# Performance work log

Measured on AMD Instinct MI355X. Metric: run time of the kernel, lower is better.

## Reference

```python
import jax, jax.numpy as jnp
import numpy as np

B, L, H, E = 2, 2048, 8, 64
S = L  # self-attention


def setup_inputs() -> dict:
    key = jax.random.key(0)
    k1, k2, k3, k4, k5 = jax.random.split(key, 5)
    return {
        "queries": jax.random.normal(k1, (B, L, H, E), dtype=jnp.float32),
        "keys": jax.random.normal(k2, (B, S, H, E), dtype=jnp.float32),
        "values": jax.random.normal(k3, (B, S, H, E), dtype=jnp.float32),
        "tau": jax.random.uniform(k4, (B, 1), dtype=jnp.float32),
        "delta": jax.random.normal(k5, (B, S), dtype=jnp.float32),
    }


def reference(queries, keys, values, tau, delta):
    # De-stationary attention: scores = (QK^T) * tau + delta, causal mask, softmax, AV
    E_ = queries.shape[-1]
    scale = 1.0 / jnp.sqrt(jnp.float32(E_))
    tau_b = tau[:, None, None, :]      # [B,1,1,1]
    delta_b = delta[:, None, None, :]  # [B,1,1,S]
    scores = jnp.einsum('blhe,bshe->bhls', queries, keys) * tau_b + delta_b  # [B,H,L,S]
    Lq, Sk = scores.shape[-2], scores.shape[-1]
    causal = jnp.triu(jnp.ones((Lq, Sk), dtype=bool), k=1)  # True = masked
    scores = jnp.where(causal[None, None], -jnp.inf, scores)
    A = jax.nn.softmax(scale * scores, axis=-1)
    V = jnp.einsum('bhls,bshd->blhd', A, values)
    return V
```

## Files before the change

kernel.cpp:

```cpp
#include <hip/hip_runtime.h>


typedef _Float16 h8 __attribute__((ext_vector_type(8)));
typedef _Float16 h2 __attribute__((ext_vector_type(2)));
typedef float f32x4 __attribute__((ext_vector_type(4)));

constexpr int Bc = 2, Lc = 2048, Hc = 8, Ec = 64, Sc = 2048;
constexpr int QT = 64, KT = 64;
constexpr int NQT = Lc / QT;
constexpr int LDK = 72;
constexpr float SCALE = 0.125f;
constexpr float LOG2E = 1.44269504088896340736f;

__device__ __forceinline__ h2 pk2(float x, float y) {
  return __builtin_bit_cast(h2, __builtin_amdgcn_cvt_pkrtz(x, y));
}

template <int CTRL>
__device__ __forceinline__ float dpp_f(float x) {
  int r = __builtin_amdgcn_update_dpp(0, __builtin_bit_cast(int, x), CTRL, 0xF, 0xF, true);
  return __builtin_bit_cast(float, r);
}
__device__ __forceinline__ float rowmax16(float x) {
  x = fmaxf(x, dpp_f<0xB1>(x));
  x = fmaxf(x, dpp_f<0x4E>(x));
  x = fmaxf(x, dpp_f<0x124>(x));
  x = fmaxf(x, dpp_f<0x128>(x));
  return x;
}

template <int CH, int EPB>
__global__ __launch_bounds__(256, 3)
void dsattn_fwd(const float* __restrict__ Qg, const float* __restrict__ Kg,
                const float* __restrict__ Vg, const float* __restrict__ taug,
                const float* __restrict__ deltag, float* __restrict__ Og,
                float* __restrict__ Opart, float* __restrict__ Mpart,
                float* __restrict__ Lpart) {
  __shared__ __align__(16) _Float16 Ks[2][KT * LDK];
  __shared__ __align__(16) _Float16 Vt[2][Ec * LDK];
  __shared__ __align__(16) _Float16 Pb[4][16 * LDK];

  const int bx = (int)blockIdx.x;
  int qt, c0;
  if (CH >= NQT) { qt = NQT - 1 - bx; c0 = 0; }
  else { qt = NQT - 1 - (bx >> 2); c0 = bx & 3; if (c0 * CH > qt) return; }
  const int nch = qt / CH + 1;
  const int ktBeg = c0 * CH;
  const int ktEnd = (qt < ktBeg + CH - 1) ? qt : (ktBeg + CH - 1);

  const int tid = threadIdx.x;
  const int wave = tid >> 6, lane = tid & 63;
  const int quad = lane >> 4, l16 = lane & 15;
  const int q0 = qt * QT;
  const int bh = (int)blockIdx.y;
  const int b = bh >> 3, h = bh & 7;

  const float ct = taug[b] * (SCALE * LOG2E);

  const int qm = q0 + (wave << 4) + l16;
  const float* qp = Qg + (((size_t)b * Lc + qm) * Hc + h) * Ec;
  h8 qfrag[2];
#pragma unroll
  for (int kk = 0; kk < 2; ++kk) {
    float4 a0 = ((const float4*)(qp + quad * 8 + kk * 32))[0];
    float4 a1 = ((const float4*)(qp + quad * 8 + kk * 32))[1];
    union { h8 v; h2 p[4]; } u;
    u.p[0] = pk2(a0.x, a0.y); u.p[1] = pk2(a0.z, a0.w);
    u.p[2] = pk2(a1.x, a1.y); u.p[3] = pk2(a1.z, a1.w);
    qfrag[kk] = u.v;
  }

  h8 onesf;
#pragma unroll
  for (int j = 0; j < 8; ++j) onesf[j] = (_Float16)1.0f;

  f32x4 Oacc[4], Osum;
#pragma unroll
  for (int nt = 0; nt < 4; ++nt) Oacc[nt] = (f32x4){0.f, 0.f, 0.f, 0.f};
  Osum = (f32x4){0.f, 0.f, 0.f, 0.f};
  float mrow[4];
#pragma unroll
  for (int r = 0; r < 4; ++r) mrow[r] = -1e30f;

  const int srow = tid >> 2;
  const int sec = (tid & 3) << 4;
  const int vrp = ((tid >> 3) + 4 * (tid & 7)) & 31;
  const int ve8 = (tid & 7) << 3;

  _Float16* pb = &Pb[wave][0];
  float dcur[4];

  {
    const int kb = ktBeg * KT;
    const float* kp = Kg + (((size_t)b * Sc + kb + srow) * Hc + h) * Ec + sec;
    float4 c0v = ((const float4*)kp)[0], c1v = ((const float4*)kp)[1];
    float4 c2v = ((const float4*)kp)[2], c3v = ((const float4*)kp)[3];
    const float* vp0 = Vg + (((size_t)b * Sc + kb + 2 * vrp) * Hc + h) * Ec + ve8;
    const float* vp1 = vp0 + Hc * Ec;
    float4 r00 = ((const float4*)vp0)[0], r01 = ((const float4*)vp0)[1];
    float4 r10 = ((const float4*)vp1)[0], r11 = ((const float4*)vp1)[1];
#pragma unroll
    for (int nt = 0; nt < 4; ++nt)
      dcur[nt] = deltag[(size_t)b * Sc + kb + nt * 16 + l16] * (SCALE * LOG2E);
    union { h8 v; h2 p[4]; } w0, w1;
    w0.p[0] = pk2(c0v.x, c0v.y); w0.p[1] = pk2(c0v.z, c0v.w);
    w0.p[2] = pk2(c1v.x, c1v.y); w0.p[3] = pk2(c1v.z, c1v.w);
    w1.p[0] = pk2(c2v.x, c2v.y); w1.p[1] = pk2(c2v.z, c2v.w);
    w1.p[2] = pk2(c3v.x, c3v.y); w1.p[3] = pk2(c3v.z, c3v.w);
    *(h8*)&Ks[0][srow * LDK + sec] = w0.v;
    *(h8*)&Ks[0][srow * LDK + sec + 8] = w1.v;
    const float e0[8] = {r00.x, r00.y, r00.z, r00.w, r01.x, r01.y, r01.z, r01.w};
    const float e1[8] = {r10.x, r10.y, r10.z, r10.w, r11.x, r11.y, r11.z, r11.w};
#pragma unroll
    for (int j = 0; j < 8; ++j)
      *(h2*)&Vt[0][(ve8 + j) * LDK + 2 * vrp] = pk2(e0[j], e1[j]);
  }

  for (int kt = ktBeg; kt <= ktEnd; ++kt) {
    const int cur = (kt - ktBeg) & 1;
    const bool pf = (kt < ktEnd);

    float4 kn0, kn1, kn2, kn3, vn00, vn01, vn10, vn11;
    float dn[4];
    if (pf) {
      const int nb = (kt + 1) * KT;
      const float* kp = Kg + (((size_t)b * Sc + nb + srow) * Hc + h) * Ec + sec;
      kn0 = ((const float4*)kp)[0]; kn1 = ((const float4*)kp)[1];
      kn2 = ((const float4*)kp)[2]; kn3 = ((const float4*)kp)[3];
      const float* vp0 = Vg + (((size_t)b * Sc + nb + 2 * vrp) * Hc + h) * Ec + ve8;
      const float* vp1 = vp0 + Hc * Ec;
      vn00 = ((const float4*)vp0)[0]; vn01 = ((const float4*)vp0)[1];
      vn10 = ((const float4*)vp1)[0]; vn11 = ((const float4*)vp1)[1];
#pragma unroll
      for (int nt = 0; nt < 4; ++nt)
        dn[nt] = deltag[(size_t)b * Sc + nb + nt * 16 + l16];
    }

    __syncthreads();

    f32x4 Sacc[4];
#pragma unroll
    for (int nt = 0; nt < 4; ++nt) Sacc[nt] = (f32x4){0.f, 0.f, 0.f, 0.f};
#pragma unroll
    for (int kk = 0; kk < 2; ++kk) {
#pragma unroll
      for (int nt = 0; nt < 4; ++nt) {
        h8 bf = *(const h8*)&Ks[cur][(nt * 16 + l16) * LDK + quad * 8 + kk * 32];
        Sacc[nt] = __builtin_amdgcn_mfma_f32_16x16x32_f16(qfrag[kk], bf, Sacc[nt], 0, 0, 0);
      }
    }

    const int kbase = kt * KT;
    const int qr0 = q0 + (wave << 4) + (quad << 2);
    const bool diag = (kt == qt);
    float sv[4][4];
#pragma unroll
    for (int nt = 0; nt < 4; ++nt) {
      const int key = kbase + nt * 16 + l16;
#pragma unroll
      for (int r = 0; r < 4; ++r) {
        float s = Sacc[nt][r] * ct + dcur[nt];
        sv[nt][r] = (!diag || key <= qr0 + r) ? s : -1e30f;
      }
    }

    float alpha[4];
#pragma unroll
    for (int r = 0; r < 4; ++r) {
      float t = fmaxf(fmaxf(sv[0][r], sv[1][r]), fmaxf(sv[2][r], sv[3][r]));
      t = rowmax16(t);
      float mn = fmaxf(mrow[r], t);
      alpha[r] = __builtin_amdgcn_exp2f(mrow[r] - mn);
      mrow[r] = mn;
    }
#pragma unroll
    for (int nt = 0; nt < 4; ++nt)
#pragma unroll
      for (int r = 0; r < 4; ++r)
        sv[nt][r] = __builtin_amdgcn_exp2f(sv[nt][r] - mrow[r]);

#pragma unroll
    for (int nt = 0; nt < 4; ++nt)
#pragma unroll
      for (int r = 0; r < 4; ++r) Oacc[nt][r] *= alpha[r];
#pragma unroll
    for (int r = 0; r < 4; ++r) Osum[r] *= alpha[r];

    {
      const int lo = l16 & 1;
      const int base = (lo ? 32 : 0) + (l16 & ~1);
#pragma unroll
      for (int r = 0; r < 4; ++r) {
        float o0 = dpp_f<0xB1>(sv[0][r]);
        float o1 = dpp_f<0xB1>(sv[1][r]);
        float o2 = dpp_f<0xB1>(sv[2][r]);
        float o3 = dpp_f<0xB1>(sv[3][r]);
        h2 d0 = pk2(lo ? o2 : sv[0][r], lo ? sv[2][r] : o0);
        h2 d1 = pk2(lo ? o3 : sv[1][r], lo ? sv[3][r] : o1);
        _Float16* pp = &pb[((quad << 2) + r) * LDK + base];
        *(h2*)pp = d0;
        *(h2*)(pp + 16) = d1;
      }
    }
    asm volatile("s_waitcnt lgkmcnt(0)" ::: "memory");

#pragma unroll
    for (int kk = 0; kk < 2; ++kk) {
      h8 af = *(const h8*)&pb[l16 * LDK + quad * 8 + kk * 32];
#pragma unroll
      for (int nt = 0; nt < 4; ++nt) {
        h8 vf = *(const h8*)&Vt[cur][(nt * 16 + l16) * LDK + quad * 8 + kk * 32];
        Oacc[nt] = __builtin_amdgcn_mfma_f32_16x16x32_f16(af, vf, Oacc[nt], 0, 0, 0);
      }
      Osum = __builtin_amdgcn_mfma_f32_16x16x32_f16(af, onesf, Osum, 0, 0, 0);
    }

    if (pf) {
      _Float16* ksn = &Ks[cur ^ 1][0];
      _Float16* vtn = &Vt[cur ^ 1][0];
      union { h8 v; h2 p[4]; } w0, w1;
      w0.p[0] = pk2(kn0.x, kn0.y); w0.p[1] = pk2(kn0.z, kn0.w);
      w0.p[2] = pk2(kn1.x, kn1.y); w0.p[3] = pk2(kn1.z, kn1.w);
      w1.p[0] = pk2(kn2.x, kn2.y); w1.p[1] = pk2(kn2.z, kn2.w);
      w1.p[2] = pk2(kn3.x, kn3.y); w1.p[3] = pk2(kn3.z, kn3.w);
      *(h8*)&ksn[srow * LDK + sec] = w0.v;
      *(h8*)&ksn[srow * LDK + sec + 8] = w1.v;
      const float e0[8] = {vn00.x, vn00.y, vn00.z, vn00.w, vn01.x, vn01.y, vn01.z, vn01.w};
      const float e1[8] = {vn10.x, vn10.y, vn10.z, vn10.w, vn11.x, vn11.y, vn11.z, vn11.w};
#pragma unroll
      for (int j = 0; j < 8; ++j)
        *(h2*)&vtn[(ve8 + j) * LDK + 2 * vrp] = pk2(e0[j], e1[j]);
#pragma unroll
      for (int nt = 0; nt < 4; ++nt) dcur[nt] = dn[nt] * (SCALE * LOG2E);
    }
  }

  if (nch == 1) {
#pragma unroll
    for (int r = 0; r < 4; ++r) {
      const int qrow = q0 + (wave << 4) + (quad << 2) + r;
      const float inv = 1.0f / Osum[r];
      float* op = Og + (((size_t)b * Lc + qrow) * Hc + h) * Ec;
#pragma unroll
      for (int nt = 0; nt < 4; ++nt) op[nt * 16 + l16] = Oacc[nt][r] * inv;
    }
  } else {
    const int g = qt / CH, rem = qt - g * CH;
    const int pre = qt + CH * (g * (g - 1) / 2) + rem * g;
    const int e = bh * EPB + pre + c0;
    float* op = Opart + (size_t)e * (QT * Ec);
#pragma unroll
    for (int r = 0; r < 4; ++r) {
      const int row = (wave << 4) + (quad << 2) + r;
#pragma unroll
      for (int nt = 0; nt < 4; ++nt)
        op[row * Ec + nt * 16 + l16] = Oacc[nt][r];
      if (l16 == 0) {
        Mpart[e * QT + row] = mrow[r];
        Lpart[e * QT + row] = Osum[r];
      }
    }
  }
}

template <int CH, int EPB>
__global__ __launch_bounds__(256, 4)
void dsattn_comb(const float* __restrict__ Opart, const float* __restrict__ Mpart,
                 const float* __restrict__ Lpart, float* __restrict__ Og) {
  const int qt = CH + (int)blockIdx.x;
  const int bh = (int)blockIdx.y;
  const int b = bh >> 3, h = bh & 7;
  const int nch = qt / CH + 1;
  const int row = threadIdx.x >> 2;
  const int colg = (threadIdx.x & 3) << 4;

  const int g = qt / CH, rem = qt - g * CH;
  const int pre = qt + CH * (g * (g - 1) / 2) + rem * g;
  const int e0 = bh * EPB + pre;

  float ms[4];
  float M = -1e30f;
  for (int c = 0; c < nch; ++c) {
    ms[c] = Mpart[(e0 + c) * QT + row];
    M = fmaxf(M, ms[c]);
  }
  float acc[16];
#pragma unroll
  for (int i = 0; i < 16; ++i) acc[i] = 0.f;
  float l = 0.f;
  for (int c = 0; c < nch; ++c) {
    const float w = __builtin_amdgcn_exp2f(ms[c] - M);
    l += w * Lpart[(e0 + c) * QT + row];
    const float* op = Opart + (size_t)(e0 + c) * (QT * Ec) + row * Ec + colg;
#pragma unroll
    for (int i = 0; i < 4; ++i) {
      float4 v = ((const float4*)op)[i];
      acc[4 * i + 0] += w * v.x; acc[4 * i + 1] += w * v.y;
      acc[4 * i + 2] += w * v.z; acc[4 * i + 3] += w * v.w;
    }
  }
  const float inv = 1.0f / l;
  const int qrow = qt * QT + row;
  float* out = Og + (((size_t)b * Lc + qrow) * Hc + h) * Ec + colg;
#pragma unroll
  for (int i = 0; i < 4; ++i) {
    float4 v;
    v.x = acc[4 * i + 0] * inv; v.y = acc[4 * i + 1] * inv;
    v.z = acc[4 * i + 2] * inv; v.w = acc[4 * i + 3] * inv;
    ((float4*)out)[i] = v;
  }
}

extern "C" void kernel_launch(void* const* d_in, const int* in_sizes, int n_in,
                              void* d_out, int out_size, void* d_ws, size_t ws_size,
                              hipStream_t stream) {
  const float* Q = (const float*)d_in[0];
  const float* K = (const float*)d_in[1];
  const float* V = (const float*)d_in[2];
  const float* tau = (const float*)d_in[3];
  const float* delta = (const float*)d_in[4];
  float* O = (float*)d_out;

  constexpr int CH = 8;
  constexpr int EPB = 80;
  constexpr int TOT_E = Bc * Hc * EPB;
  const size_t need = (size_t)TOT_E * QT * Ec * 4 + 2 * (size_t)TOT_E * QT * 4;

  if (ws_size >= need) {
    float* Opart = (float*)d_ws;
    float* Mpart = Opart + (size_t)TOT_E * QT * Ec;
    float* Lpart = Mpart + (size_t)TOT_E * QT;
    dim3 g1(NQT * 4, Bc * Hc);
    dsattn_fwd<CH, EPB><<<g1, 256, 0, stream>>>(Q, K, V, tau, delta, O,
                                                Opart, Mpart, Lpart);
    dim3 g2(NQT - CH, Bc * Hc);
    dsattn_comb<CH, EPB><<<g2, 256, 0, stream>>>(Opart, Mpart, Lpart, O);
  } else {
    dim3 g1(NQT, Bc * Hc);
    dsattn_fwd<NQT, NQT><<<g1, 256, 0, stream>>>(Q, K, V, tau, delta, O,
                                                 nullptr, nullptr, nullptr);
  }
}
```

Before: 129.6 us.

## Double query tile to 128 rows per block, two fragments per wave

Each block now handles 128 query rows, with each wave owning two 16-row fragments. Every K/V tile staged in LDS is therefore reused across twice as many queries, and each K fragment read feeds two MFMAs. Waves whose rows lie entirely before a key tile skip that tile's compute, and the split-K chunking and combine kernel are rewritten for the new tile size. The cost is more registers, occupancy dropping from three blocks to two, and half as many blocks (fewer q tiles), which may underfill the GPU.

```diff
diff --git a/kernel.cpp b/kernel.cpp
--- a/kernel.cpp
+++ b/kernel.cpp
@@ -6,8 +6,9 @@
 typedef float f32x4 __attribute__((ext_vector_type(4)));
 
 constexpr int Bc = 2, Lc = 2048, Hc = 8, Ec = 64, Sc = 2048;
-constexpr int QT = 64, KT = 64;
-constexpr int NQT = Lc / QT;
+constexpr int QTL = 128;
+constexpr int NQT = Lc / QTL;
+constexpr int KT = 64;
 constexpr int LDK = 72;
 constexpr float SCALE = 0.125f;
 constexpr float LOG2E = 1.44269504088896340736f;
@@ -15,7 +16,6 @@
 __device__ __forceinline__ h2 pk2(float x, float y) {
   return __builtin_bit_cast(h2, __builtin_amdgcn_cvt_pkrtz(x, y));
 }
-
 template <int CTRL>
 __device__ __forceinline__ float dpp_f(float x) {
   int r = __builtin_amdgcn_update_dpp(0, __builtin_bit_cast(int, x), CTRL, 0xF, 0xF, true);
@@ -29,8 +29,8 @@
   return x;
 }
 
-template <int CH, int EPB>
-__global__ __launch_bounds__(256, 3)
+template <int CH_IT, int EPB>
+__global__ __launch_bounds__(256, 2)
 void dsattn_fwd(const float* __restrict__ Qg, const float* __restrict__ Kg,
                 const float* __restrict__ Vg, const float* __restrict__ taug,
                 const float* __restrict__ deltag, float* __restrict__ Og,
@@ -38,49 +38,56 @@
                 float* __restrict__ Lpart) {
   __shared__ __align__(16) _Float16 Ks[2][KT * LDK];
   __shared__ __align__(16) _Float16 Vt[2][Ec * LDK];
-  __shared__ __align__(16) _Float16 Pb[4][16 * LDK];
+  __shared__ __align__(16) _Float16 Pb[4][32 * LDK];
 
   const int bx = (int)blockIdx.x;
   int qt, c0;
-  if (CH >= NQT) { qt = NQT - 1 - bx; c0 = 0; }
-  else { qt = NQT - 1 - (bx >> 2); c0 = bx & 3; if (c0 * CH > qt) return; }
-  const int nch = qt / CH + 1;
-  const int ktBeg = c0 * CH;
-  const int ktEnd = (qt < ktBeg + CH - 1) ? qt : (ktBeg + CH - 1);
+  if (CH_IT >= 2 * NQT) { qt = NQT - 1 - bx; c0 = 0; }
+  else { qt = NQT - 1 - (bx >> 2); c0 = bx & 3; }
+  const int ntiles = 2 * qt + 2;
+  const int nch = (ntiles + CH_IT - 1) / CH_IT;
+  if (c0 >= nch) return;
+
+  const int ktBeg = c0 * CH_IT;
+  const int ktEnd = min(ktBeg + CH_IT - 1, ntiles - 1);
 
   const int tid = threadIdx.x;
   const int wave = tid >> 6, lane = tid & 63;
   const int quad = lane >> 4, l16 = lane & 15;
-  const int q0 = qt * QT;
+  const int q0 = qt * QTL;
   const int bh = (int)blockIdx.y;
   const int b = bh >> 3, h = bh & 7;
-
   const float ct = taug[b] * (SCALE * LOG2E);
 
-  const int qm = q0 + (wave << 4) + l16;
-  const float* qp = Qg + (((size_t)b * Lc + qm) * Hc + h) * Ec;
-  h8 qfrag[2];
-#pragma unroll
-  for (int kk = 0; kk < 2; ++kk) {
-    float4 a0 = ((const float4*)(qp + quad * 8 + kk * 32))[0];
-    float4 a1 = ((const float4*)(qp + quad * 8 + kk * 32))[1];
-    union { h8 v; h2 p[4]; } u;
-    u.p[0] = pk2(a0.x, a0.y); u.p[1] = pk2(a0.z, a0.w);
-    u.p[2] = pk2(a1.x, a1.y); u.p[3] = pk2(a1.z, a1.w);
-    qfrag[kk] = u.v;
-  }
+  h8 qfrag[2][2];
+#pragma unroll
+  for (int f = 0; f < 2; ++f)
+#pragma unroll
+    for (int kk = 0; kk < 2; ++kk) {
+      const float* qp = Qg + (((size_t)b * Lc + q0 + 32 * wave + 16 * f + l16) * Hc + h) * Ec
+                       + quad * 8 + kk * 32;
+      const float4* p = (const float4*)qp;
+      union { h8 v; h2 c[4]; } u;
+      float4 a0 = p[0], a1 = p[1];
+      u.c[0] = pk2(a0.x, a0.y); u.c[1] = pk2(a0.z, a0.w);
+      u.c[2] = pk2(a1.x, a1.y); u.c[3] = pk2(a1.z, a1.w);
+      qfrag[f][kk] = u.v;
+    }
 
   h8 onesf;
 #pragma unroll
   for (int j = 0; j < 8; ++j) onesf[j] = (_Float16)1.0f;
 
-  f32x4 Oacc[4], Osum;
-#pragma unroll
-  for (int nt = 0; nt < 4; ++nt) Oacc[nt] = (f32x4){0.f, 0.f, 0.f, 0.f};
-  Osum = (f32x4){0.f, 0.f, 0.f, 0.f};
-  float mrow[4];
-#pragma unroll
-  for (int r = 0; r < 4; ++r) mrow[r] = -1e30f;
+  f32x4 Oacc[2][4], Osum[2];
+  float mrow[2][4];
+#pragma unroll
+  for (int f = 0; f < 2; ++f) {
+#pragma unroll
+    for (int nt = 0; nt < 4; ++nt) Oacc[f][nt] = (f32x4){0.f, 0.f, 0.f, 0.f};
+    Osum[f] = (f32x4){0.f, 0.f, 0.f, 0.f};
+#pragma unroll
+    for (int r = 0; r < 4; ++r) mrow[f][r] = -1e30f;
+  }
 
   const int srow = tid >> 2;
   const int sec = (tid & 3) << 4;
@@ -88,6 +95,8 @@
   const int ve8 = (tid & 7) << 3;
 
   _Float16* pb = &Pb[wave][0];
+  const int lo = l16 & 1;
+  const int pbase = (lo ? 32 : 0) + (l16 & ~1);
   float dcur[4];
 
   {
@@ -102,11 +111,11 @@
 #pragma unroll
     for (int nt = 0; nt < 4; ++nt)
       dcur[nt] = deltag[(size_t)b * Sc + kb + nt * 16 + l16] * (SCALE * LOG2E);
-    union { h8 v; h2 p[4]; } w0, w1;
-    w0.p[0] = pk2(c0v.x, c0v.y); w0.p[1] = pk2(c0v.z, c0v.w);
-    w0.p[2] = pk2(c1v.x, c1v.y); w0.p[3] = pk2(c1v.z, c1v.w);
-    w1.p[0] = pk2(c2v.x, c2v.y); w1.p[1] = pk2(c2v.z, c2v.w);
-    w1.p[2] = pk2(c3v.x, c3v.y); w1.p[3] = pk2(c3v.z, c3v.w);
+    union { h8 v; h2 c[4]; } w0, w1;
+    w0.c[0] = pk2(c0v.x, c0v.y); w0.c[1] = pk2(c0v.z, c0v.w);
+    w0.c[2] = pk2(c1v.x, c1v.y); w0.c[3] = pk2(c1v.z, c1v.w);
+    w1.c[0] = pk2(c2v.x, c2v.y); w1.c[1] = pk2(c2v.z, c2v.w);
+    w1.c[2] = pk2(c3v.x, c3v.y); w1.c[3] = pk2(c3v.z, c3v.w);
     *(h8*)&Ks[0][srow * LDK + sec] = w0.v;
     *(h8*)&Ks[0][srow * LDK + sec + 8] = w1.v;
     const float e0[8] = {r00.x, r00.y, r00.z, r00.w, r01.x, r01.y, r01.z, r01.w};
@@ -119,6 +128,7 @@
   for (int kt = ktBeg; kt <= ktEnd; ++kt) {
     const int cur = (kt - ktBeg) & 1;
     const bool pf = (kt < ktEnd);
+    const int kbase = kt * KT;
 
     float4 kn0, kn1, kn2, kn3, vn00, vn01, vn10, vn11;
     float dn[4];
@@ -138,91 +148,103 @@
 
     __syncthreads();
 
-    f32x4 Sacc[4];
-#pragma unroll
-    for (int nt = 0; nt < 4; ++nt) Sacc[nt] = (f32x4){0.f, 0.f, 0.f, 0.f};
-#pragma unroll
-    for (int kk = 0; kk < 2; ++kk) {
-#pragma unroll
-      for (int nt = 0; nt < 4; ++nt) {
-        h8 bf = *(const h8*)&Ks[cur][(nt * 16 + l16) * LDK + quad * 8 + kk * 32];
-        Sacc[nt] = __builtin_amdgcn_mfma_f32_16x16x32_f16(qfrag[kk], bf, Sacc[nt], 0, 0, 0);
-      }
-    }
-
-    const int kbase = kt * KT;
-    const int qr0 = q0 + (wave << 4) + (quad << 2);
-    const bool diag = (kt == qt);
-    float sv[4][4];
-#pragma unroll
-    for (int nt = 0; nt < 4; ++nt) {
-      const int key = kbase + nt * 16 + l16;
-#pragma unroll
-      for (int r = 0; r < 4; ++r) {
-        float s = Sacc[nt][r] * ct + dcur[nt];
-        sv[nt][r] = (!diag || key <= qr0 + r) ? s : -1e30f;
-      }
-    }
-
-    float alpha[4];
-#pragma unroll
-    for (int r = 0; r < 4; ++r) {
-      float t = fmaxf(fmaxf(sv[0][r], sv[1][r]), fmaxf(sv[2][r], sv[3][r]));
-      t = rowmax16(t);
-      float mn = fmaxf(mrow[r], t);
-      alpha[r] = __builtin_amdgcn_exp2f(mrow[r] - mn);
-      mrow[r] = mn;
-    }
-#pragma unroll
-    for (int nt = 0; nt < 4; ++nt)
-#pragma unroll
-      for (int r = 0; r < 4; ++r)
-        sv[nt][r] = __builtin_amdgcn_exp2f(sv[nt][r] - mrow[r]);
-
-#pragma unroll
-    for (int nt = 0; nt < 4; ++nt)
-#pragma unroll
-      for (int r = 0; r < 4; ++r) Oacc[nt][r] *= alpha[r];
-#pragma unroll
-    for (int r = 0; r < 4; ++r) Osum[r] *= alpha[r];
-
-    {
-      const int lo = l16 & 1;
-      const int base = (lo ? 32 : 0) + (l16 & ~1);
-#pragma unroll
-      for (int r = 0; r < 4; ++r) {
-        float o0 = dpp_f<0xB1>(sv[0][r]);
-        float o1 = dpp_f<0xB1>(sv[1][r]);
-        float o2 = dpp_f<0xB1>(sv[2][r]);
-        float o3 = dpp_f<0xB1>(sv[3][r]);
-        h2 d0 = pk2(lo ? o2 : sv[0][r], lo ? sv[2][r] : o0);
-        h2 d1 = pk2(lo ? o3 : sv[1][r], lo ? sv[3][r] : o1);
-        _Float16* pp = &pb[((quad << 2) + r) * LDK + base];
-        *(h2*)pp = d0;
-        *(h2*)(pp + 16) = d1;
-      }
-    }
-    asm volatile("s_waitcnt lgkmcnt(0)" ::: "memory");
-
-#pragma unroll
-    for (int kk = 0; kk < 2; ++kk) {
-      h8 af = *(const h8*)&pb[l16 * LDK + quad * 8 + kk * 32];
-#pragma unroll
-      for (int nt = 0; nt < 4; ++nt) {
-        h8 vf = *(const h8*)&Vt[cur][(nt * 16 + l16) * LDK + quad * 8 + kk * 32];
-        Oacc[nt] = __builtin_amdgcn_mfma_f32_16x16x32_f16(af, vf, Oacc[nt], 0, 0, 0);
-      }
-      Osum = __builtin_amdgcn_mfma_f32_16x16x32_f16(af, onesf, Osum, 0, 0, 0);
+    const int wtop = q0 + 32 * wave + 31;
+    if (kbase <= wtop) {
+      f32x4 Sacc[2][4];
+#pragma unroll
+      for (int f = 0; f < 2; ++f)
+#pragma unroll
+        for (int nt = 0; nt < 4; ++nt) Sacc[f][nt] = (f32x4){0.f, 0.f, 0.f, 0.f};
+#pragma unroll
+      for (int kk = 0; kk < 2; ++kk) {
+        h8 bf[4];
+#pragma unroll
+        for (int nt = 0; nt < 4; ++nt)
+          bf[nt] = *(const h8*)&Ks[cur][(nt * 16 + l16) * LDK + quad * 8 + kk * 32];
+#pragma unroll
+        for (int f = 0; f < 2; ++f)
+#pragma unroll
+          for (int nt = 0; nt < 4; ++nt)
+            Sacc[f][nt] = __builtin_amdgcn_mfma_f32_16x16x32_f16(qfrag[f][kk], bf[nt], Sacc[f][nt], 0, 0, 0);
+      }
+
+#pragma unroll
+      for (int f = 0; f < 2; ++f) {
+        const int fr0 = q0 + 32 * wave + 16 * f;
+        float sv[4][4];
+#pragma unroll
+        for (int nt = 0; nt < 4; ++nt)
+#pragma unroll
+          for (int r = 0; r < 4; ++r)
+            sv[nt][r] = Sacc[f][nt][r] * ct + dcur[nt];
+        if (kbase + 63 > fr0) {
+#pragma unroll
+          for (int nt = 0; nt < 4; ++nt) {
+            const int key = kbase + nt * 16 + l16;
+#pragma unroll
+            for (int r = 0; r < 4; ++r)
+              if (key > fr0 + quad * 4 + r) sv[nt][r] = -1e30f;
+          }
+        }
+#pragma unroll
+        for (int r = 0; r < 4; ++r) {
+          float tm = fmaxf(fmaxf(sv[0][r], sv[1][r]), fmaxf(sv[2][r], sv[3][r]));
+          tm = rowmax16(tm);
+          float mn = fmaxf(mrow[f][r], tm);
+          float alpha = __builtin_amdgcn_exp2f(mrow[f][r] - mn);
+          mrow[f][r] = mn;
+#pragma unroll
+          for (int nt = 0; nt < 4; ++nt)
+            sv[nt][r] = __builtin_amdgcn_exp2f(sv[nt][r] - mn);
+          Osum[f][r] *= alpha;
+#pragma unroll
+          for (int nt = 0; nt < 4; ++nt) Oacc[f][nt][r] *= alpha;
+        }
+#pragma unroll
+        for (int r = 0; r < 4; ++r) {
+          float o0 = dpp_f<0xB1>(sv[0][r]);
+          float o1 = dpp_f<0xB1>(sv[1][r]);
+          float o2 = dpp_f<0xB1>(sv[2][r]);
+          float o3 = dpp_f<0xB1>(sv[3][r]);
+          h2 d0 = lo ? pk2(o2, sv[2][r]) : pk2(sv[0][r], o0);
+          h2 d1 = lo ? pk2(o3, sv[3][r]) : pk2(sv[1][r], o1);
+          _Float16* pp = &pb[(16 * f + (quad << 2) + r) * LDK + pbase];
+          *(h2*)pp = d0;
+          *(h2*)(pp + 16) = d1;
+        }
+      }
+      asm volatile("s_waitcnt lgkmcnt(0)" ::: "memory");
+
+      h8 af[2][2];
+#pragma unroll
+      for (int f = 0; f < 2; ++f)
+#pragma unroll
+        for (int kk = 0; kk < 2; ++kk)
+          af[f][kk] = *(const h8*)&pb[(16 * f + l16) * LDK + quad * 8 + kk * 32];
+
+#pragma unroll
+      for (int kk = 0; kk < 2; ++kk) {
+#pragma unroll
+        for (int nt = 0; nt < 4; ++nt) {
+          h8 vf = *(const h8*)&Vt[cur][(nt * 16 + l16) * LDK + quad * 8 + kk * 32];
+#pragma unroll
+          for (int f = 0; f < 2; ++f)
+            Oacc[f][nt] = __builtin_amdgcn_mfma_f32_16x16x32_f16(af[f][kk], vf, Oacc[f][nt], 0, 0, 0);
+        }
+#pragma unroll
+        for (int f = 0; f < 2; ++f)
+          Osum[f] = __builtin_amdgcn_mfma_f32_16x16x32_f16(af[f][kk], onesf, Osum[f], 0, 0, 0);
+      }
     }
 
     if (pf) {
       _Float16* ksn = &Ks[cur ^ 1][0];
       _Float16* vtn = &Vt[cur ^ 1][0];
-      union { h8 v; h2 p[4]; } w0, w1;
-      w0.p[0] = pk2(kn0.x, kn0.y); w0.p[1] = pk2(kn0.z, kn0.w);
-      w0.p[2] = pk2(kn1.x, kn1.y); w0.p[3] = pk2(kn1.z, kn1.w);
-      w1.p[0] = pk2(kn2.x, kn2.y); w1.p[1] = pk2(kn2.z, kn2.w);
-      w1.p[2] = pk2(kn3.x, kn3.y); w1.p[3] = pk2(kn3.z, kn3.w);
+      union { h8 v; h2 c[4]; } w0, w1;
+      w0.c[0] = pk2(kn0.x, kn0.y); w0.c[1] = pk2(kn0.z, kn0.w);
+      w0.c[2] = pk2(kn1.x, kn1.y); w0.c[3] = pk2(kn1.z, kn1.w);
+      w1.c[0] = pk2(kn2.x, kn2.y); w1.c[1] = pk2(kn2.z, kn2.w);
+      w1.c[2] = pk2(kn3.x, kn3.y); w1.c[3] = pk2(kn3.z, kn3.w);
       *(h8*)&ksn[srow * LDK + sec] = w0.v;
       *(h8*)&ksn[srow * LDK + sec + 8] = w1.v;
       const float e0[8] = {vn00.x, vn00.y, vn00.z, vn00.w, vn01.x, vn01.y, vn01.z, vn01.w};
@@ -237,77 +259,70 @@
 
   if (nch == 1) {
 #pragma unroll
-    for (int r = 0; r < 4; ++r) {
-      const int qrow = q0 + (wave << 4) + (quad << 2) + r;
-      const float inv = 1.0f / Osum[r];
-      float* op = Og + (((size_t)b * Lc + qrow) * Hc + h) * Ec;
-#pragma unroll
-      for (int nt = 0; nt < 4; ++nt) op[nt * 16 + l16] = Oacc[nt][r] * inv;
-    }
+    for (int f = 0; f < 2; ++f)
+#pragma unroll
+      for (int r = 0; r < 4; ++r) {
+        const int qrow = q0 + 32 * wave + 16 * f + (quad << 2) + r;
+        const float inv = 1.0f / Osum[f][r];
+        float* op = Og + (((size_t)b * Lc + qrow) * Hc + h) * Ec;
+#pragma unroll
+        for (int nt = 0; nt < 4; ++nt) op[nt * 16 + l16] = Oacc[f][nt][r] * inv;
+      }
   } else {
-    const int g = qt / CH, rem = qt - g * CH;
-    const int pre = qt + CH * (g * (g - 1) / 2) + rem * g;
+    const int g = qt >> 2, rem = qt & 3;
+    const int pre = qt + 4 * (g * (g - 1) / 2) + rem * g;
     const int e = bh * EPB + pre + c0;
-    float* op = Opart + (size_t)e * (QT * Ec);
-#pragma unroll
-    for (int r = 0; r < 4; ++r) {
-      const int row = (wave << 4) + (quad << 2) + r;
-#pragma unroll
-      for (int nt = 0; nt < 4; ++nt)
-        op[row * Ec + nt * 16 + l16] = Oacc[nt][r];
-      if (l16 == 0) {
-        Mpart[e * QT + row] = mrow[r];
-        Lpart[e * QT + row] = Osum[r];
-      }
-    }
-  }
-}
-
-template <int CH, int EPB>
+    float* op = Opart + (size_t)e * (QTL * Ec);
+#pragma unroll
+    for (int f = 0; f < 2; ++f)
+#pragma unroll
+      for (int r = 0; r < 4; ++r) {
+        const int row = 32 * wave + 16 * f + (quad << 2) + r;
+#pragma unroll
+        for (int nt = 0; nt < 4; ++nt) op[row * Ec + nt * 16 + l16] = Oacc[f][nt][r];
+        if (l16 == 0) {
+          Mpart[e * QTL + row] = mrow[f][r];
+          Lpart[e * QTL + row] = Osum[f][r];
+        }
+      }
+  }
+}
+
+template <int EPB>
 __global__ __launch_bounds__(256, 4)
 void dsattn_comb(const float* __restrict__ Opart, const float* __restrict__ Mpart,
                  const float* __restrict__ Lpart, float* __restrict__ Og) {
-  const int qt = CH + (int)blockIdx.x;
+  const int qt = 4 + (int)blockIdx.x;
   const int bh = (int)blockIdx.y;
   const int b = bh >> 3, h = bh & 7;
-  const int nch = qt / CH + 1;
-  const int row = threadIdx.x >> 2;
-  const int colg = (threadIdx.x & 3) << 4;
-
-  const int g = qt / CH, rem = qt - g * CH;
-  const int pre = qt + CH * (g * (g - 1) / 2) + rem * g;
+  const int nch = (qt >> 2) + 1;
+  const int g = qt >> 2, rem = qt & 3;
+  const int pre = qt + 4 * (g * (g - 1) / 2) + rem * g;
   const int e0 = bh * EPB + pre;
-
-  float ms[4];
-  float M = -1e30f;
-  for (int c = 0; c < nch; ++c) {
-    ms[c] = Mpart[(e0 + c) * QT + row];
-    M = fmaxf(M, ms[c]);
-  }
-  float acc[16];
-#pragma unroll
-  for (int i = 0; i < 16; ++i) acc[i] = 0.f;
-  float l = 0.f;
-  for (int c = 0; c < nch; ++c) {
-    const float w = __builtin_amdgcn_exp2f(ms[c] - M);
-    l += w * Lpart[(e0 + c) * QT + row];
-    const float* op = Opart + (size_t)(e0 + c) * (QT * Ec) + row * Ec + colg;
-#pragma unroll
-    for (int i = 0; i < 4; ++i) {
-      float4 v = ((const float4*)op)[i];
-      acc[4 * i + 0] += w * v.x; acc[4 * i + 1] += w * v.y;
-      acc[4 * i + 2] += w * v.z; acc[4 * i + 3] += w * v.w;
-    }
-  }
-  const float inv = 1.0f / l;
-  const int qrow = qt * QT + row;
-  float* out = Og + (((size_t)b * Lc + qrow) * Hc + h) * Ec + colg;
-#pragma unroll
-  for (int i = 0; i < 4; ++i) {
-    float4 v;
-    v.x = acc[4 * i + 0] * inv; v.y = acc[4 * i + 1] * inv;
-    v.z = acc[4 * i + 2] * inv; v.w = acc[4 * i + 3] * inv;
-    ((float4*)out)[i] = v;
+  const int tid = threadIdx.x;
+  const int c4 = (tid & 15) << 2;
+
+#pragma unroll
+  for (int i = 0; i < 8; ++i) {
+    const int row = (tid >> 4) + 16 * i;
+    float ms[4];
+    float M = -1e30f;
+    for (int c = 0; c < nch; ++c) {
+      ms[c] = Mpart[(e0 + c) * QTL + row];
+      M = fmaxf(M, ms[c]);
+    }
+    float4 acc = {0.f, 0.f, 0.f, 0.f};
+    float l = 0.f;
+    for (int c = 0; c < nch; ++c) {
+      const float w = __builtin_amdgcn_exp2f(ms[c] - M);
+      l += w * Lpart[(e0 + c) * QTL + row];
+      float4 v = *(const float4*)(Opart + (size_t)(e0 + c) * (QTL * Ec) + row * Ec + c4);
+      acc.x += w * v.x; acc.y += w * v.y; acc.z += w * v.z; acc.w += w * v.w;
+    }
+    const float inv = 1.0f / l;
+    float* out = Og + (((size_t)b * Lc + qt * QTL + row) * Hc + h) * Ec + c4;
+    float4 o; o.x = acc.x * inv; o.y = acc.y * inv; o.z = acc.z * inv; o.w = acc.w * inv;
+    *(float4*)out = o;
   }
 }
 
@@ -321,23 +336,22 @@
   const float* delta = (const float*)d_in[4];
   float* O = (float*)d_out;
 
-  constexpr int CH = 8;
-  constexpr int EPB = 80;
+  constexpr int EPB = 40;
   constexpr int TOT_E = Bc * Hc * EPB;
-  const size_t need = (size_t)TOT_E * QT * Ec * 4 + 2 * (size_t)TOT_E * QT * 4;
+  const size_t need = (size_t)TOT_E * QTL * Ec * 4 + 2 * (size_t)TOT_E * QTL * 4;
 
   if (ws_size >= need) {
     float* Opart = (float*)d_ws;
-    float* Mpart = Opart + (size_t)TOT_E * QT * Ec;
-    float* Lpart = Mpart + (size_t)TOT_E * QT;
+    float* Mpart = Opart + (size_t)TOT_E * QTL * Ec;
+    float* Lpart = Mpart + (size_t)TOT_E * QTL;
     dim3 g1(NQT * 4, Bc * Hc);
-    dsattn_fwd<CH, EPB><<<g1, 256, 0, stream>>>(Q, K, V, tau, delta, O,
-                                                Opart, Mpart, Lpart);
-    dim3 g2(NQT - CH, Bc * Hc);
-    dsattn_comb<CH, EPB><<<g2, 256, 0, stream>>>(Opart, Mpart, Lpart, O);
+    dsattn_fwd<8, EPB><<<g1, 256, 0, stream>>>(Q, K, V, tau, delta, O,
+                                               Opart, Mpart, Lpart);
+    dim3 g2(NQT - 4, Bc * Hc);
+    dsattn_comb<EPB><<<g2, 256, 0, stream>>>(Opart, Mpart, Lpart, O);
   } else {
     dim3 g1(NQT, Bc * Hc);
-    dsattn_fwd<NQT, NQT><<<g1, 256, 0, stream>>>(Q, K, V, tau, delta, O,
-                                                 nullptr, nullptr, nullptr);
-  }
-}
+    dsattn_fwd<32, 1><<<g1, 256, 0, stream>>>(Q, K, V, tau, delta, O,
+                                              nullptr, nullptr, nullptr);
+  }
+}
```

Result: slower. 138.0 us (+6.5%).
